# Kernel optimization log

Hardware: AMD Instinct MI355X
Metric: run time of the kernel (lower is better)

Reference implementation:

```python
import jax, jax.numpy as jnp
import numpy as np

WS = 7        # window size
H = 32; W = 32  # input resolution
NH = 12       # num heads
HD = 32       # head dim (key_dim; attn_ratio=1 so d == key_dim)
DIM = 384
EPS = 1e-5


def _make_bias_idxs():
    # replicate itertools.product offset-insertion order: idx = |dy|*WS + |dx|
    coords = np.array(list(np.ndindex(WS, WS)))              # [N,2]
    off = np.abs(coords[:, None, :] - coords[None, :, :])    # [N,N,2]
    return jnp.asarray(off[..., 0] * WS + off[..., 1], dtype=jnp.int64)


def setup_inputs() -> dict:
    key = jax.random.key(0)
    ks = jax.random.split(key, 8)
    B = 32
    s = 0.02
    return {
        "x": jax.random.normal(ks[0], (B, H * W, DIM), jnp.float32),
        "ln1_w": jnp.ones((DIM,), jnp.float32),
        "ln1_b": jnp.zeros((DIM,), jnp.float32),
        "qkv_w": jax.random.normal(ks[1], (DIM, 3 * DIM), jnp.float32) * s,
        "qkv_b": jnp.zeros((3 * DIM,), jnp.float32),
        "proj_w": jax.random.normal(ks[2], (DIM, DIM), jnp.float32) * s,
        "proj_b": jnp.zeros((DIM,), jnp.float32),
        "attn_bias": jax.random.normal(ks[3], (NH, WS * WS), jnp.float32) * s,
        "bias_idxs": _make_bias_idxs(),
        "conv_w": jax.random.normal(ks[4], (DIM, 1, 3, 3), jnp.float32) * s,
        "bn_g": jnp.ones((DIM,), jnp.float32),
        "bn_b": jnp.zeros((DIM,), jnp.float32),
        "bn_m": jax.random.normal(ks[5], (DIM,), jnp.float32) * s,
        "bn_v": jax.random.uniform(ks[6], (DIM,), jnp.float32, 0.5, 1.5),
        "ln2_w": jnp.ones((DIM,), jnp.float32),
        "ln2_b": jnp.zeros((DIM,), jnp.float32),
        "fc1_w": jax.random.normal(ks[7], (DIM, 4 * DIM), jnp.float32) * s,
        "fc1_b": jnp.zeros((4 * DIM,), jnp.float32),
        "fc2_w": jax.random.normal(jax.random.fold_in(key, 9), (4 * DIM, DIM), jnp.float32) * s,
        "fc2_b": jnp.zeros((DIM,), jnp.float32),
    }


def _layernorm(x, w, b):
    mu = x.mean(-1, keepdims=True)
    var = x.var(-1, keepdims=True)
    return (x - mu) * jax.lax.rsqrt(var + EPS) * w + b


def reference(x, ln1_w, ln1_b, qkv_w, qkv_b, proj_w, proj_b, attn_bias,
              bias_idxs, conv_w, bn_g, bn_b, bn_m, bn_v,
              ln2_w, ln2_b, fc1_w, fc1_b, fc2_w, fc2_b):
    B, L, C = x.shape
    res = x
    # --- window partition (with bottom/right padding) ---
    pad_b = (WS - H % WS) % WS
    pad_r = (WS - W % WS) % WS
    xi = jnp.pad(x.reshape(B, H, W, C), ((0, 0), (0, pad_b), (0, pad_r), (0, 0)))
    pH, pW = H + pad_b, W + pad_r
    nh, nw = pH // WS, pW // WS
    xw = xi.reshape(B, nh, WS, nw, WS, C).transpose(0, 1, 3, 2, 4, 5)
    xw = xw.reshape(B * nh * nw, WS * WS, C)            # [Bw, N, C]
    # --- attention with gathered relative-position bias ---
    N = WS * WS
    xn = _layernorm(xw, ln1_w, ln1_b)
    qkv = (xn @ qkv_w + qkv_b).reshape(-1, N, NH, 3 * HD)
    q, k, v = qkv[..., :HD], qkv[..., HD:2 * HD], qkv[..., 2 * HD:]
    bias = attn_bias[:, bias_idxs]                       # [NH, N, N]
    attn = jnp.einsum('bnhd,bmhd->bhnm', q, k) * (HD ** -0.5) + bias[None]
    attn = jax.nn.softmax(attn, axis=-1)
    o = jnp.einsum('bhnm,bmhd->bnhd', attn, v).reshape(-1, N, NH * HD)
    o = o @ proj_w + proj_b
    # --- window reverse, crop padding ---
    o = o.reshape(B, nh, nw, WS, WS, C).transpose(0, 1, 3, 2, 4, 5)
    o = o.reshape(B, pH, pW, C)[:, :H, :W]
    x = res + o.reshape(B, L, C)
    # --- depthwise local conv + BatchNorm (eval stats) ---
    xc = x.transpose(0, 2, 1).reshape(B, C, H, W)
    xc = jax.lax.conv_general_dilated(
        xc, conv_w, (1, 1), 'SAME', feature_group_count=C,
        dimension_numbers=('NCHW', 'OIHW', 'NCHW'))
    inv = jax.lax.rsqrt(bn_v + EPS)
    xc = (xc - bn_m[None, :, None, None]) * (inv * bn_g)[None, :, None, None] \
         + bn_b[None, :, None, None]
    x = xc.reshape(B, C, L).transpose(0, 2, 1)
    # --- MLP (LN -> fc1 -> GELU -> fc2) with residual ---
    xn = _layernorm(x, ln2_w, ln2_b)
    hden = jax.nn.gelu(xn @ fc1_w + fc1_b, approximate=False)
    return x + (hden @ fc2_w + fc2_b)
```

## Files before the change

### kernel.cpp

```cpp
#include <hip/hip_runtime.h>
#include <math.h>

#define EPSF 1e-5f

#define NROW   32768
#define CDIM   384
#define N3     1152
#define FFDIM  1536

typedef unsigned short ushort_t;
typedef __attribute__((ext_vector_type(8))) short short8v;
typedef __attribute__((ext_vector_type(4))) float f32x4;

__device__ __forceinline__ float gelu_exact(float v) {
    return 0.5f * v * (1.f + erff(v * 0.70710678118654752f));
}

__device__ __forceinline__ float gelu_fast(float x) {
    float y = 1.5957691216f * x + 0.0713548162f * (x * x * x);
    return x * __builtin_amdgcn_rcpf(1.f + __expf(-y));
}

__device__ __forceinline__ ushort_t f2bf(float f) {
    union { float f; unsigned u; } v; v.f = f;
    unsigned r = v.u + 0x7fffu + ((v.u >> 16) & 1u);
    return (ushort_t)(r >> 16);
}

__device__ __forceinline__ void gload_lds16(const void* g, void* l) {
    __builtin_amdgcn_global_load_lds(
        (const __attribute__((address_space(1))) void*)g,
        (__attribute__((address_space(3))) void*)l, 16, 0, 0);
}

__global__ __launch_bounds__(256) void wt_bf16_kernel(const float* __restrict__ W,
                                                      ushort_t* __restrict__ Wt,
                                                      int K, int N) {
    __shared__ float t[32][33];
    const int bx = blockIdx.x, by = blockIdx.y;
    const int c = threadIdx.x & 31, r0 = threadIdx.x >> 5;
    #pragma unroll
    for (int i = 0; i < 4; ++i) {
        int r = r0 + i * 8;
        t[r][c] = W[(size_t)(by * 32 + r) * N + bx * 32 + c];
    }
    __syncthreads();
    #pragma unroll
    for (int i = 0; i < 4; ++i) {
        int r = r0 + i * 8;
        Wt[(size_t)(bx * 32 + r) * K + by * 32 + c] = f2bf(t[c][r]);
    }
}

__global__ __launch_bounds__(256) void padvec_kernel(
    const float* __restrict__ ln1_b, const float* __restrict__ qkv_w,
    const float* __restrict__ qkv_b, ushort_t* __restrict__ padvec)
{
    int j = blockIdx.x * 256 + threadIdx.x;
    if (j >= N3) return;
    float acc = qkv_b[j];
    for (int k = 0; k < CDIM; ++k) acc = fmaf(ln1_b[k], qkv_w[k * N3 + j], acc);
    padvec[j] = f2bf(acc);
}

__global__ __launch_bounds__(256) void ln_bf16_kernel(
    const float* __restrict__ src, const float* __restrict__ w,
    const float* __restrict__ b, ushort_t* __restrict__ dst)
{
    const int row  = blockIdx.x * 4 + (threadIdx.x >> 6);
    const int lane = threadIdx.x & 63;
    const float* p = src + (size_t)row * CDIM;
    float vals[6];
    float s1 = 0.f, s2 = 0.f;
    #pragma unroll
    for (int i = 0; i < 6; ++i) {
        float v = p[lane + 64 * i];
        vals[i] = v; s1 += v; s2 += v * v;
    }
    #pragma unroll
    for (int off = 32; off > 0; off >>= 1) {
        s1 += __shfl_xor(s1, off);
        s2 += __shfl_xor(s2, off);
    }
    float mu = s1 * (1.f / CDIM);
    float rs = rsqrtf(s2 * (1.f / CDIM) - mu * mu + EPSF);
    ushort_t* q = dst + (size_t)row * CDIM;
    #pragma unroll
    for (int i = 0; i < 6; ++i) {
        int k = lane + 64 * i;
        q[k] = f2bf((vals[i] - mu) * rs * w[k] + b[k]);
    }
}

template<int EPI>
__global__ __launch_bounds__(256) void gemm_bf16_kernel(
    const ushort_t* __restrict__ A, const ushort_t* __restrict__ Bt,
    const float* __restrict__ bias, void* __restrict__ outv,
    const float* __restrict__ resid, int Nn, int K)
{
    __shared__ __align__(16) char raw[34816];
    ushort_t (*As)[64] = (ushort_t(*)[64])raw;
    ushort_t (*Bs)[64] = (ushort_t(*)[64])(raw + 16384);

    const int tid  = threadIdx.x;
    const int lane = tid & 63;
    const int wv   = tid >> 6;
    const int wm   = (wv & 1) * 64, wn = (wv >> 1) * 64;

    const int nbx = gridDim.x;
    const int nwg = nbx * gridDim.y;
    const int id  = blockIdx.y * nbx + blockIdx.x;
    const int cpx = nwg >> 3;
    const int swz = (id & 7) * cpx + (id >> 3);
    const int bn0 = (swz % nbx) * 128;
    const int bm0 = (swz / nbx) * 128;

    const int g_row = lane >> 3;
    const int g_col = ((lane & 7) ^ g_row) * 8;

    f32x4 acc[4][4] = {};

    const int cl = lane & 15;
    const int lg = lane >> 4;
    const int sx = (cl & 7) << 4;

    const char* Ab = raw;
    const char* Bb = raw + 16384;

    for (int kt = 0; kt < K; kt += 64) {
        if (kt) __syncthreads();
        #pragma unroll
        for (int i = 0; i < 4; ++i) {
            const int r = wv * 32 + i * 8;
            gload_lds16(A  + (size_t)(bm0 + r + g_row) * K + kt + g_col, &As[r][0]);
            gload_lds16(Bt + (size_t)(bn0 + r + g_row) * K + kt + g_col, &Bs[r][0]);
        }
        __syncthreads();
        #pragma unroll
        for (int kb = 0; kb < 2; ++kb) {
            const int cob = (kb * 64 + lg * 16) ^ sx;
            short8v a[4], b[4];
            #pragma unroll
            for (int mi = 0; mi < 4; ++mi)
                a[mi] = *(const short8v*)(Ab + (wm + mi * 16 + cl) * 128 + cob);
            #pragma unroll
            for (int ni = 0; ni < 4; ++ni)
                b[ni] = *(const short8v*)(Bb + (wn + ni * 16 + cl) * 128 + cob);
            #pragma unroll
            for (int mi = 0; mi < 4; ++mi)
                #pragma unroll
                for (int ni = 0; ni < 4; ++ni)
                    acc[mi][ni] = __builtin_amdgcn_mfma_f32_16x16x32_bf16(
                        a[mi], b[ni], acc[mi][ni], 0, 0, 0);
        }
    }
    __syncthreads();

    float* Cw = (float*)(raw + wv * 8704);
    const int ecol = cl * 4;
    const float4 bb = *(const float4*)(bias + bn0 + wn + ecol);

    #pragma unroll
    for (int half = 0; half < 2; ++half) {
        #pragma unroll
        for (int mi2 = 0; mi2 < 2; ++mi2) {
            #pragma unroll
            for (int ni = 0; ni < 4; ++ni) {
                #pragma unroll
                for (int r = 0; r < 4; ++r)
                    Cw[(mi2 * 16 + lg * 4 + r) * 68 + ni * 16 + cl] =
                        acc[half * 2 + mi2][ni][r];
            }
        }
        __syncthreads();
        #pragma unroll
        for (int i = 0; i < 8; ++i) {
            const int lrow = i * 4 + lg;
            const int grow = bm0 + wm + half * 32 + lrow;
            float4 v = *(const float4*)&Cw[lrow * 68 + ecol];
            v.x += bb.x; v.y += bb.y; v.z += bb.z; v.w += bb.w;
            size_t off = (size_t)grow * Nn + bn0 + wn + ecol;
            if (EPI == 0) {
                ushort4 pk = { f2bf(v.x), f2bf(v.y), f2bf(v.z), f2bf(v.w) };
                *(ushort4*)((ushort_t*)outv + off) = pk;
            } else if (EPI == 1) {
                ushort4 pk = { f2bf(gelu_fast(v.x)), f2bf(gelu_fast(v.y)),
                               f2bf(gelu_fast(v.z)), f2bf(gelu_fast(v.w)) };
                *(ushort4*)((ushort_t*)outv + off) = pk;
            } else {
                float4 r0 = *(const float4*)(resid + off);
                v.x += r0.x; v.y += r0.y; v.z += r0.z; v.w += r0.w;
                *(float4*)((float*)outv + off) = v;
            }
        }
        __syncthreads();
    }
}

__global__ __launch_bounds__(256) void attn_kernel(
    const ushort_t* __restrict__ qkv, const ushort_t* __restrict__ padvec,
    const float* __restrict__ attn_bias, const int* __restrict__ bias_idxs,
    ushort_t* __restrict__ o)
{
    const int w = blockIdx.x / 12;
    const int h = blockIdx.x % 12;
    __shared__ ushort_t Qs[64][40];
    __shared__ ushort_t Ks[64][40];
    __shared__ ushort_t Vts[32][72];
    __shared__ ushort_t Ps[64][72];
    __shared__ float    browl[49];
    __shared__ int      simgl[49];
    const int tid  = threadIdx.x;
    const int lane = tid & 63;
    const int wv   = tid >> 6;
    const int cl   = lane & 15;
    const int lg   = lane >> 4;

    if (tid < 49) {
        int b  = w / 25, wi = w % 25;
        int gh = (wi / 5) * 7 + tid / 7;
        int gw = (wi % 5) * 7 + tid % 7;
        simgl[tid] = (gh < 32 && gw < 32) ? (b * 1024 + gh * 32 + gw) : -1;
        browl[tid] = attn_bias[h * 49 + tid];
    }

    for (int e = tid; e < 64 * 12; e += 256) {
        int t = e / 12, j = e % 12;
        uint4 val = make_uint4(0u, 0u, 0u, 0u);
        if (t < 49) {
            int b  = w / 25, wi = w % 25;
            int gh = (wi / 5) * 7 + t / 7;
            int gw = (wi % 5) * 7 + t % 7;
            const ushort_t* src = (gh < 32 && gw < 32)
                ? qkv + (size_t)(b * 1024 + gh * 32 + gw) * N3 + h * 96 + j * 8
                : padvec + h * 96 + j * 8;
            val = *(const uint4*)src;
        }
        if (j < 4)      *(uint4*)&Qs[t][j * 8] = val;
        else if (j < 8) *(uint4*)&Ks[t][(j - 4) * 8] = val;
        else {
            int d0 = (j - 8) * 8;
            unsigned uu[4] = {val.x, val.y, val.z, val.w};
            #pragma unroll
            for (int ii = 0; ii < 4; ++ii) {
                Vts[d0 + 2 * ii + 0][t] = (ushort_t)(uu[ii] & 0xffffu);
                Vts[d0 + 2 * ii + 1][t] = (ushort_t)(uu[ii] >> 16);
            }
        }
    }
    __syncthreads();

    const int q = wv * 16 + cl;
    short8v qf = *(const short8v*)&Qs[q][lg * 8];
    f32x4 st[4];
    #pragma unroll
    for (int mi = 0; mi < 4; ++mi) {
        short8v kf = *(const short8v*)&Ks[mi * 16 + cl][lg * 8];
        f32x4 z = {};
        st[mi] = __builtin_amdgcn_mfma_f32_16x16x32_bf16(kf, qf, z, 0, 0, 0);
    }

    float sv[4][4];
    float m = -1e30f;
    #pragma unroll
    for (int mi = 0; mi < 4; ++mi)
        #pragma unroll
        for (int r = 0; r < 4; ++r) {
            int key = mi * 16 + lg * 4 + r;
            float bb = (q < 49 && key < 49)
                     ? browl[bias_idxs[q * 49 + key]] : -1e30f;
            float s = st[mi][r] * 0.17677669529663687f + bb;
            sv[mi][r] = s;
            m = fmaxf(m, s);
        }
    m = fmaxf(m, __shfl_xor(m, 16));
    m = fmaxf(m, __shfl_xor(m, 32));
    float sum = 0.f;
    #pragma unroll
    for (int mi = 0; mi < 4; ++mi)
        #pragma unroll
        for (int r = 0; r < 4; ++r) {
            float p = __expf(sv[mi][r] - m);
            sv[mi][r] = p;
            sum += p;
        }
    sum += __shfl_xor(sum, 16);
    sum += __shfl_xor(sum, 32);
    const float inv = 1.f / sum;

    #pragma unroll
    for (int mi = 0; mi < 4; ++mi) {
        uint2 pk;
        pk.x = (unsigned)f2bf(sv[mi][0] * inv) | ((unsigned)f2bf(sv[mi][1] * inv) << 16);
        pk.y = (unsigned)f2bf(sv[mi][2] * inv) | ((unsigned)f2bf(sv[mi][3] * inv) << 16);
        *(uint2*)&Ps[q][mi * 16 + lg * 4] = pk;
    }

    f32x4 oacc[2] = {};
    #pragma unroll
    for (int kb = 0; kb < 2; ++kb) {
        short8v pa = *(const short8v*)&Ps[q][kb * 32 + lg * 8];
        #pragma unroll
        for (int ni = 0; ni < 2; ++ni) {
            short8v vb = *(const short8v*)&Vts[ni * 16 + cl][kb * 32 + lg * 8];
            oacc[ni] = __builtin_amdgcn_mfma_f32_16x16x32_bf16(pa, vb, oacc[ni], 0, 0, 0);
        }
    }

    #pragma unroll
    for (int ni = 0; ni < 2; ++ni) {
        int d = h * 32 + ni * 16 + cl;
        #pragma unroll
        for (int r = 0; r < 4; ++r) {
            int q2 = wv * 16 + lg * 4 + r;
            if (q2 < 49) {
                int si = simgl[q2];
                if (si >= 0) o[(size_t)si * CDIM + d] = f2bf(oacc[ni][r]);
            }
        }
    }
}

__global__ __launch_bounds__(256) void conv_bn_kernel(
    const float* __restrict__ xin, const float* __restrict__ cw,
    const float* __restrict__ bn_g, const float* __restrict__ bn_b,
    const float* __restrict__ bn_m, const float* __restrict__ bn_v,
    float* __restrict__ xout)
{
    __shared__ float wsm[9 * 384];
    for (int i = threadIdx.x; i < 9 * 384; i += 256) {
        int c = i / 9, wi = i % 9;
        wsm[wi * 384 + c] = cw[i];
    }
    __syncthreads();

    int gid = blockIdx.x * 256 + threadIdx.x;
    int c4 = gid % 96;
    int t  = gid / 96;
    int w  = t % 32; t /= 32;
    int h  = t % 32;
    int b  = t / 32;
    int c0 = c4 * 4;

    float4 acc = make_float4(0.f, 0.f, 0.f, 0.f);
    #pragma unroll
    for (int dh = -1; dh <= 1; ++dh) {
        int hh = h + dh;
        if (hh < 0 || hh >= 32) continue;
        #pragma unroll
        for (int dw = -1; dw <= 1; ++dw) {
            int ww = w + dw;
            if (ww < 0 || ww >= 32) continue;
            float4 xv = *(const float4*)(xin + ((size_t)(b * 1024 + hh * 32 + ww)) * CDIM + c0);
            float4 wv = *(const float4*)&wsm[((dh + 1) * 3 + (dw + 1)) * 384 + c0];
            acc.x = fmaf(xv.x, wv.x, acc.x);
            acc.y = fmaf(xv.y, wv.y, acc.y);
            acc.z = fmaf(xv.z, wv.z, acc.z);
            acc.w = fmaf(xv.w, wv.w, acc.w);
        }
    }
    float4 o;
    float sc;
    sc = rsqrtf(bn_v[c0 + 0] + EPSF) * bn_g[c0 + 0]; o.x = (acc.x - bn_m[c0 + 0]) * sc + bn_b[c0 + 0];
    sc = rsqrtf(bn_v[c0 + 1] + EPSF) * bn_g[c0 + 1]; o.y = (acc.y - bn_m[c0 + 1]) * sc + bn_b[c0 + 1];
    sc = rsqrtf(bn_v[c0 + 2] + EPSF) * bn_g[c0 + 2]; o.z = (acc.z - bn_m[c0 + 2]) * sc + bn_b[c0 + 2];
    sc = rsqrtf(bn_v[c0 + 3] + EPSF) * bn_g[c0 + 3]; o.w = (acc.w - bn_m[c0 + 3]) * sc + bn_b[c0 + 3];
    *(float4*)(xout + (size_t)gid * 4) = o;
}

extern "C" void kernel_launch(void* const* d_in, const int* in_sizes, int n_in,
                              void* d_out, int out_size, void* d_ws, size_t ws_size,
                              hipStream_t stream) {
    const float* x         = (const float*)d_in[0];
    const float* ln1_w     = (const float*)d_in[1];
    const float* ln1_b     = (const float*)d_in[2];
    const float* qkv_w     = (const float*)d_in[3];
    const float* qkv_b     = (const float*)d_in[4];
    const float* proj_w    = (const float*)d_in[5];
    const float* proj_b    = (const float*)d_in[6];
    const float* attn_bias = (const float*)d_in[7];
    const int*   bias_idxs = (const int*)d_in[8];
    const float* conv_w    = (const float*)d_in[9];
    const float* bn_g      = (const float*)d_in[10];
    const float* bn_b      = (const float*)d_in[11];
    const float* bn_m      = (const float*)d_in[12];
    const float* bn_v      = (const float*)d_in[13];
    const float* ln2_w     = (const float*)d_in[14];
    const float* ln2_b     = (const float*)d_in[15];
    const float* fc1_w     = (const float*)d_in[16];
    const float* fc1_b     = (const float*)d_in[17];
    const float* fc2_w     = (const float*)d_in[18];
    const float* fc2_b     = (const float*)d_in[19];
    float* out = (float*)d_out;

    char* ws = (char*)d_ws;
    ushort_t* A1    = (ushort_t*)(ws + 0);
    ushort_t* oimg  = (ushort_t*)(ws + 0);
    ushort_t* A2    = (ushort_t*)(ws + 0);
    ushort_t* qkvb  = (ushort_t*)(ws + 25165824ULL);
    float*    x1    = (float*)(ws + 25165824ULL);
    ushort_t* hbuf  = (ushort_t*)(ws + 25165824ULL);
    ushort_t* wtqkv = (ushort_t*)(ws + 176160768ULL);
    ushort_t* wtprj = (ushort_t*)(ws + 177045504ULL);
    ushort_t* wtfc1 = (ushort_t*)(ws + 177340416ULL);
    ushort_t* wtfc2 = (ushort_t*)(ws + 178520064ULL);
    ushort_t* pvec  = (ushort_t*)(ws + 179699712ULL);

    wt_bf16_kernel<<<dim3(36, 12), 256, 0, stream>>>(qkv_w,  wtqkv, 384, 1152);
    wt_bf16_kernel<<<dim3(12, 12), 256, 0, stream>>>(proj_w, wtprj, 384, 384);
    wt_bf16_kernel<<<dim3(48, 12), 256, 0, stream>>>(fc1_w,  wtfc1, 384, 1536);
    wt_bf16_kernel<<<dim3(12, 48), 256, 0, stream>>>(fc2_w,  wtfc2, 1536, 384);
    padvec_kernel<<<5, 256, 0, stream>>>(ln1_b, qkv_w, qkv_b, pvec);
    ln_bf16_kernel<<<8192, 256, 0, stream>>>(x, ln1_w, ln1_b, A1);
    gemm_bf16_kernel<0><<<dim3(9, 256), 256, 0, stream>>>(
        A1, wtqkv, qkv_b, qkvb, nullptr, N3, CDIM);
    attn_kernel<<<9600, 256, 0, stream>>>(qkvb, pvec, attn_bias, bias_idxs, oimg);
    gemm_bf16_kernel<2><<<dim3(3, 256), 256, 0, stream>>>(
        oimg, wtprj, proj_b, x1, x, CDIM, CDIM);
    conv_bn_kernel<<<12288, 256, 0, stream>>>(x1, conv_w, bn_g, bn_b, bn_m, bn_v, out);
    ln_bf16_kernel<<<8192, 256, 0, stream>>>(out, ln2_w, ln2_b, A2);
    gemm_bf16_kernel<1><<<dim3(12, 256), 256, 0, stream>>>(
        A2, wtfc1, fc1_b, hbuf, nullptr, FFDIM, CDIM);
    gemm_bf16_kernel<2><<<dim3(3, 256), 256, 0, stream>>>(
        hbuf, wtfc2, fc2_b, out, out, CDIM, FFDIM);
}
```

Before: 452.9 us.

## Double-buffer GEMM LDS tiles, template K, direct residual epilogue, merge prep kernels

The GEMM now ping-pongs between two 32KB LDS buffers, issuing the async global-to-LDS load for the next K tile before computing the current one. This cuts the sync count per K step and hides load latency. K becomes a template parameter so the loop is compile-time sized. The residual epilogue skips the LDS staging and writes scalar floats straight from the accumulators, and the five weight-prep launches are merged into one kernel. The larger 64KB LDS footprint may lower occupancy, and the scalar residual stores are less coalesced.

```diff
diff --git a/kernel.cpp b/kernel.cpp
--- a/kernel.cpp
+++ b/kernel.cpp
@@ -12,10 +12,6 @@
 typedef __attribute__((ext_vector_type(8))) short short8v;
 typedef __attribute__((ext_vector_type(4))) float f32x4;
 
-__device__ __forceinline__ float gelu_exact(float v) {
-    return 0.5f * v * (1.f + erff(v * 0.70710678118654752f));
-}
-
 __device__ __forceinline__ float gelu_fast(float x) {
     float y = 1.5957691216f * x + 0.0713548162f * (x * x * x);
     return x * __builtin_amdgcn_rcpf(1.f + __expf(-y));
@@ -33,11 +29,11 @@
         (__attribute__((address_space(3))) void*)l, 16, 0, 0);
 }
 
-__global__ __launch_bounds__(256) void wt_bf16_kernel(const float* __restrict__ W,
-                                                      ushort_t* __restrict__ Wt,
-                                                      int K, int N) {
-    __shared__ float t[32][33];
-    const int bx = blockIdx.x, by = blockIdx.y;
+__device__ __forceinline__ void wt_body(const float* __restrict__ W,
+                                        ushort_t* __restrict__ Wt,
+                                        int K, int N, int idx, int nbx,
+                                        float (*t)[33]) {
+    const int bx = idx % nbx, by = idx / nbx;
     const int c = threadIdx.x & 31, r0 = threadIdx.x >> 5;
     #pragma unroll
     for (int i = 0; i < 4; ++i) {
@@ -52,15 +48,28 @@
     }
 }
 
-__global__ __launch_bounds__(256) void padvec_kernel(
-    const float* __restrict__ ln1_b, const float* __restrict__ qkv_w,
-    const float* __restrict__ qkv_b, ushort_t* __restrict__ padvec)
+__global__ __launch_bounds__(256) void prep_kernel(
+    const float* __restrict__ qkv_w, const float* __restrict__ proj_w,
+    const float* __restrict__ fc1_w, const float* __restrict__ fc2_w,
+    const float* __restrict__ ln1_b, const float* __restrict__ qkv_b,
+    ushort_t* __restrict__ wtqkv, ushort_t* __restrict__ wtprj,
+    ushort_t* __restrict__ wtfc1, ushort_t* __restrict__ wtfc2,
+    ushort_t* __restrict__ padvec)
 {
-    int j = blockIdx.x * 256 + threadIdx.x;
-    if (j >= N3) return;
-    float acc = qkv_b[j];
-    for (int k = 0; k < CDIM; ++k) acc = fmaf(ln1_b[k], qkv_w[k * N3 + j], acc);
-    padvec[j] = f2bf(acc);
+    __shared__ float t[32][33];
+    const int bid = blockIdx.x;
+    if (bid < 432)       wt_body(qkv_w,  wtqkv, 384, 1152, bid,        36, t);
+    else if (bid < 576)  wt_body(proj_w, wtprj, 384, 384,  bid - 432,  12, t);
+    else if (bid < 1152) wt_body(fc1_w,  wtfc1, 384, 1536, bid - 576,  48, t);
+    else if (bid < 1728) wt_body(fc2_w,  wtfc2, 1536, 384, bid - 1152, 12, t);
+    else {
+        int j = (bid - 1728) * 256 + threadIdx.x;
+        if (j < N3) {
+            float acc = qkv_b[j];
+            for (int k = 0; k < CDIM; ++k) acc = fmaf(ln1_b[k], qkv_w[k * N3 + j], acc);
+            padvec[j] = f2bf(acc);
+        }
+    }
 }
 
 __global__ __launch_bounds__(256) void ln_bf16_kernel(
@@ -92,15 +101,13 @@
     }
 }
 
-template<int EPI>
+template<int EPI, int K>
 __global__ __launch_bounds__(256) void gemm_bf16_kernel(
     const ushort_t* __restrict__ A, const ushort_t* __restrict__ Bt,
     const float* __restrict__ bias, void* __restrict__ outv,
-    const float* __restrict__ resid, int Nn, int K)
+    const float* __restrict__ resid, int Nn)
 {
-    __shared__ __align__(16) char raw[34816];
-    ushort_t (*As)[64] = (ushort_t(*)[64])raw;
-    ushort_t (*Bs)[64] = (ushort_t(*)[64])(raw + 16384);
+    __shared__ __align__(16) char raw[65536];
 
     const int tid  = threadIdx.x;
     const int lane = tid & 63;
@@ -124,18 +131,17 @@
     const int lg = lane >> 4;
     const int sx = (cl & 7) << 4;
 
-    const char* Ab = raw;
-    const char* Bb = raw + 16384;
-
-    for (int kt = 0; kt < K; kt += 64) {
-        if (kt) __syncthreads();
+    auto stage = [&](char* base, int kt) {
         #pragma unroll
         for (int i = 0; i < 4; ++i) {
             const int r = wv * 32 + i * 8;
-            gload_lds16(A  + (size_t)(bm0 + r + g_row) * K + kt + g_col, &As[r][0]);
-            gload_lds16(Bt + (size_t)(bn0 + r + g_row) * K + kt + g_col, &Bs[r][0]);
-        }
-        __syncthreads();
+            gload_lds16(A  + (size_t)(bm0 + r + g_row) * K + kt + g_col, base + r * 128);
+            gload_lds16(Bt + (size_t)(bn0 + r + g_row) * K + kt + g_col, base + 16384 + r * 128);
+        }
+    };
+    auto compute = [&](const char* base) {
+        const char* Ab = base;
+        const char* Bb = base + 16384;
         #pragma unroll
         for (int kb = 0; kb < 2; ++kb) {
             const int cob = (kb * 64 + lg * 16) ^ sx;
@@ -153,47 +159,74 @@
                     acc[mi][ni] = __builtin_amdgcn_mfma_f32_16x16x32_bf16(
                         a[mi], b[ni], acc[mi][ni], 0, 0, 0);
         }
-    }
+    };
+
+    char* buf0 = raw;
+    char* buf1 = raw + 32768;
+    constexpr int NT = K / 64;
+
+    stage(buf0, 0);
     __syncthreads();
-
-    float* Cw = (float*)(raw + wv * 8704);
-    const int ecol = cl * 4;
-    const float4 bb = *(const float4*)(bias + bn0 + wn + ecol);
-
-    #pragma unroll
-    for (int half = 0; half < 2; ++half) {
-        #pragma unroll
-        for (int mi2 = 0; mi2 < 2; ++mi2) {
-            #pragma unroll
-            for (int ni = 0; ni < 4; ++ni) {
+    #pragma unroll 1
+    for (int t = 0; t < NT; t += 2) {
+        stage(buf1, (t + 1) * 64);
+        compute(buf0);
+        __syncthreads();
+        if (t + 2 < NT) stage(buf0, (t + 2) * 64);
+        compute(buf1);
+        __syncthreads();
+    }
+
+    const int rq = lg * 4;
+
+    if (EPI == 2) {
+        #pragma unroll
+        for (int ni = 0; ni < 4; ++ni) {
+            const int col = bn0 + wn + ni * 16 + cl;
+            const float bs = bias[col];
+            #pragma unroll
+            for (int mi = 0; mi < 4; ++mi) {
+                const int row0 = bm0 + wm + mi * 16 + rq;
                 #pragma unroll
-                for (int r = 0; r < 4; ++r)
-                    Cw[(mi2 * 16 + lg * 4 + r) * 68 + ni * 16 + cl] =
-                        acc[half * 2 + mi2][ni][r];
+                for (int r = 0; r < 4; ++r) {
+                    size_t off = (size_t)(row0 + r) * Nn + col;
+                    ((float*)outv)[off] = acc[mi][ni][r] + bs + resid[off];
+                }
             }
         }
-        __syncthreads();
-        #pragma unroll
-        for (int i = 0; i < 8; ++i) {
-            const int lrow = i * 4 + lg;
-            const int grow = bm0 + wm + half * 32 + lrow;
-            float4 v = *(const float4*)&Cw[lrow * 68 + ecol];
-            v.x += bb.x; v.y += bb.y; v.z += bb.z; v.w += bb.w;
-            size_t off = (size_t)grow * Nn + bn0 + wn + ecol;
-            if (EPI == 0) {
+    } else {
+        float* Cw = (float*)(raw + wv * 8704);
+        const int ecol = cl * 4;
+        const float4 bb = *(const float4*)(bias + bn0 + wn + ecol);
+        #pragma unroll
+        for (int half = 0; half < 2; ++half) {
+            #pragma unroll
+            for (int mi2 = 0; mi2 < 2; ++mi2) {
+                #pragma unroll
+                for (int ni = 0; ni < 4; ++ni) {
+                    #pragma unroll
+                    for (int r = 0; r < 4; ++r)
+                        Cw[(mi2 * 16 + rq + r) * 68 + ni * 16 + cl] =
+                            acc[half * 2 + mi2][ni][r];
+                }
+            }
+            __syncthreads();
+            #pragma unroll
+            for (int i = 0; i < 8; ++i) {
+                const int lrow = i * 4 + lg;
+                const int grow = bm0 + wm + half * 32 + lrow;
+                float4 v = *(const float4*)&Cw[lrow * 68 + ecol];
+                v.x += bb.x; v.y += bb.y; v.z += bb.z; v.w += bb.w;
+                size_t off = (size_t)grow * Nn + bn0 + wn + ecol;
+                if (EPI == 1) {
+                    v.x = gelu_fast(v.x); v.y = gelu_fast(v.y);
+                    v.z = gelu_fast(v.z); v.w = gelu_fast(v.w);
+                }
                 ushort4 pk = { f2bf(v.x), f2bf(v.y), f2bf(v.z), f2bf(v.w) };
                 *(ushort4*)((ushort_t*)outv + off) = pk;
-            } else if (EPI == 1) {
-                ushort4 pk = { f2bf(gelu_fast(v.x)), f2bf(gelu_fast(v.y)),
-                               f2bf(gelu_fast(v.z)), f2bf(gelu_fast(v.w)) };
-                *(ushort4*)((ushort_t*)outv + off) = pk;
-            } else {
-                float4 r0 = *(const float4*)(resid + off);
-                v.x += r0.x; v.y += r0.y; v.z += r0.z; v.w += r0.w;
-                *(float4*)((float*)outv + off) = v;
             }
-        }
-        __syncthreads();
+            __syncthreads();
+        }
     }
 }
 
@@ -406,21 +439,18 @@
     ushort_t* wtfc2 = (ushort_t*)(ws + 178520064ULL);
     ushort_t* pvec  = (ushort_t*)(ws + 179699712ULL);
 
-    wt_bf16_kernel<<<dim3(36, 12), 256, 0, stream>>>(qkv_w,  wtqkv, 384, 1152);
-    wt_bf16_kernel<<<dim3(12, 12), 256, 0, stream>>>(proj_w, wtprj, 384, 384);
-    wt_bf16_kernel<<<dim3(48, 12), 256, 0, stream>>>(fc1_w,  wtfc1, 384, 1536);
-    wt_bf16_kernel<<<dim3(12, 48), 256, 0, stream>>>(fc2_w,  wtfc2, 1536, 384);
-    padvec_kernel<<<5, 256, 0, stream>>>(ln1_b, qkv_w, qkv_b, pvec);
+    prep_kernel<<<1733, 256, 0, stream>>>(qkv_w, proj_w, fc1_w, fc2_w, ln1_b, qkv_b,
+                                          wtqkv, wtprj, wtfc1, wtfc2, pvec);
     ln_bf16_kernel<<<8192, 256, 0, stream>>>(x, ln1_w, ln1_b, A1);
-    gemm_bf16_kernel<0><<<dim3(9, 256), 256, 0, stream>>>(
-        A1, wtqkv, qkv_b, qkvb, nullptr, N3, CDIM);
+    gemm_bf16_kernel<0, 384><<<dim3(9, 256), 256, 0, stream>>>(
+        A1, wtqkv, qkv_b, qkvb, nullptr, N3);
     attn_kernel<<<9600, 256, 0, stream>>>(qkvb, pvec, attn_bias, bias_idxs, oimg);
-    gemm_bf16_kernel<2><<<dim3(3, 256), 256, 0, stream>>>(
-        oimg, wtprj, proj_b, x1, x, CDIM, CDIM);
+    gemm_bf16_kernel<2, 384><<<dim3(3, 256), 256, 0, stream>>>(
+        oimg, wtprj, proj_b, x1, x, CDIM);
     conv_bn_kernel<<<12288, 256, 0, stream>>>(x1, conv_w, bn_g, bn_b, bn_m, bn_v, out);
     ln_bf16_kernel<<<8192, 256, 0, stream>>>(out, ln2_w, ln2_b, A2);
-    gemm_bf16_kernel<1><<<dim3(12, 256), 256, 0, stream>>>(
-        A2, wtfc1, fc1_b, hbuf, nullptr, FFDIM, CDIM);
-    gemm_bf16_kernel<2><<<dim3(3, 256), 256, 0, stream>>>(
-        hbuf, wtfc2, fc2_b, out, out, CDIM, FFDIM);
-}
+    gemm_bf16_kernel<1, 384><<<dim3(12, 256), 256, 0, stream>>>(
+        A2, wtfc1, fc1_b, hbuf, nullptr, FFDIM);
+    gemm_bf16_kernel<2, 1536><<<dim3(3, 256), 256, 0, stream>>>(
+        hbuf, wtfc2, fc2_b, out, out, CDIM);
+}
```

Measured after the change: 442.8 us. 2.2% less time.
